# Kernel optimization log

Hardware: AMD Instinct MI355X
Metric: run time of the kernel (lower is better)

Reference implementation:

```python
import jax, jax.numpy as jnp
import numpy as np

B, T, EPROJS, DUNITS, ATT_DIM = 32, 2048, 512, 512, 512
ACONV_CHANS, ACONV_FILT = 32, 100
SCALING = 2.0


def _lin(k, fan_in, fan_out):
    k1, k2 = jax.random.split(k)
    lim = 1.0 / np.sqrt(fan_in)
    w = jax.random.uniform(k1, (fan_in, fan_out), minval=-lim, maxval=lim, dtype=jnp.float32)
    b = jax.random.uniform(k2, (fan_out,), minval=-lim, maxval=lim, dtype=jnp.float32)
    return w, b


def setup_inputs() -> dict:
    key = jax.random.key(0)
    ks = jax.random.split(key, 16)
    W_w, W_b = _lin(ks[0], DUNITS, ATT_DIM)
    V_w, V_b = _lin(ks[1], EPROJS, ATT_DIM)
    U_w, U_b = _lin(ks[2], DUNITS, ATT_DIM)
    g_w, g_b = _lin(ks[3], ATT_DIM, 1)
    K = 2 * ACONV_FILT + 1
    lim = 1.0 / np.sqrt(K)
    conv_w = jax.random.uniform(ks[4], (ACONV_CHANS, 1, K), minval=-lim, maxval=lim, dtype=jnp.float32)
    lim = 1.0 / np.sqrt(ATT_DIM)
    W_ih = jax.random.uniform(ks[5], (4 * ATT_DIM, ACONV_CHANS), minval=-lim, maxval=lim, dtype=jnp.float32)
    W_hh = jax.random.uniform(ks[6], (4 * ATT_DIM, ATT_DIM), minval=-lim, maxval=lim, dtype=jnp.float32)
    b_ih = jax.random.uniform(ks[7], (4 * ATT_DIM,), minval=-lim, maxval=lim, dtype=jnp.float32)
    b_hh = jax.random.uniform(ks[8], (4 * ATT_DIM,), minval=-lim, maxval=lim, dtype=jnp.float32)
    enc_hs_pad = jax.random.normal(ks[9], (B, T, EPROJS), dtype=jnp.float32)
    enc_hs_len = jax.random.randint(ks[10], (B,), T // 2, T + 1, dtype=jnp.int32)
    dec_z = jax.random.normal(ks[11], (B, DUNITS), dtype=jnp.float32)
    att_prev = jax.random.uniform(ks[12], (B, T), dtype=jnp.float32)
    att_h = jax.random.normal(ks[13], (B, ATT_DIM), dtype=jnp.float32)
    att_c = jax.random.normal(ks[14], (B, ATT_DIM), dtype=jnp.float32)
    return dict(enc_hs_pad=enc_hs_pad, enc_hs_len=enc_hs_len, dec_z=dec_z,
                att_prev=att_prev, att_h=att_h, att_c=att_c,
                W_w=W_w, W_b=W_b, V_w=V_w, V_b=V_b, U_w=U_w, U_b=U_b,
                g_w=g_w, g_b=g_b, conv_w=conv_w,
                W_ih=W_ih, W_hh=W_hh, b_ih=b_ih, b_hh=b_hh)


def reference(enc_hs_pad, enc_hs_len, dec_z, att_prev, att_h, att_c,
              W_w, W_b, V_w, V_b, U_w, U_b, g_w, g_b, conv_w,
              W_ih, W_hh, b_ih, b_hh):
    # pre-computed encoder projection: (B, T, att_dim)
    pre = jnp.einsum('bte,ea->bta', enc_hs_pad, V_w) + V_b
    # location conv over previous attention weights: (B, C, T)
    conv = jax.lax.conv_general_dilated(att_prev[:, None, :], conv_w,
                                        window_strides=(1,),
                                        padding=[(ACONV_FILT, ACONV_FILT)],
                                        dimension_numbers=('NCH', 'OIH', 'NCH'))
    feat = jnp.max(jax.nn.relu(conv), axis=-1)  # (B, C): max-pool over time
    # LSTMCell (torch gate order: i, f, g, o)
    gates = feat @ W_ih.T + b_ih + att_h @ W_hh.T + b_hh
    i, f, g, o = jnp.split(gates, 4, axis=-1)
    c_new = jax.nn.sigmoid(f) * att_c + jax.nn.sigmoid(i) * jnp.tanh(g)
    h_new = jax.nn.sigmoid(o) * jnp.tanh(c_new)
    # additive score
    dec_proj = dec_z @ U_w + U_b            # (B, att_dim)
    wh = h_new @ W_w + W_b                  # (B, att_dim)
    e = jnp.tanh(wh[:, None, :] + pre + dec_proj[:, None, :])  # (B, T, att_dim)
    score = jnp.einsum('bta,a->bt', e, g_w[:, 0]) + g_b[0]     # (B, T)
    mask = jnp.arange(T)[None, :] >= enc_hs_len[:, None]
    score = jnp.where(mask, jnp.asarray(-1e30, score.dtype), score)
    w = jax.nn.softmax(SCALING * score, axis=1)
    c_v = jnp.einsum('bte,bt->be', enc_hs_pad, w)  # (B, eprojs)
    return c_v, w, h_new, c_new
```

## Files before the change

kernel.cpp:

```cpp
#include <hip/hip_runtime.h>
#include <math.h>

#define BB 32
#define TT_SEQ 2048
#define EPROJS 512
#define ATT 512
#define NCH 32
#define FILT 100
#define KCONV 201
#define G4 2048

typedef unsigned short ushort_t;
typedef unsigned int uint_t;
typedef __attribute__((ext_vector_type(8))) short bf16x8_t;
typedef __attribute__((ext_vector_type(4))) float f32x4_t;

__device__ inline ushort_t f2bf(float f) {
    uint_t u = __float_as_uint(f);
    uint_t r = (u + 0x7fffu + ((u >> 16) & 1u)) >> 16;
    return (ushort_t)r;
}

__device__ inline float tanh_fast(float x) {
    float e = __expf(2.0f * x);
    return 1.0f - 2.0f / (e + 1.0f);
}

__global__ __launch_bounds__(256) void k_conv(const float* __restrict__ att_prev,
                                              const float* __restrict__ conv_w,
                                              float* __restrict__ feat) {
    int b = blockIdx.x >> 5;
    int c = blockIdx.x & 31;
    __shared__ __align__(16) float row[TT_SEQ + 2 * FILT + 8];
    __shared__ float red[4];
    for (int i = threadIdx.x; i < TT_SEQ + 2 * FILT + 8; i += 256) {
        int t = i - FILT;
        row[i] = (t >= 0 && t < TT_SEQ) ? att_prev[b * TT_SEQ + t] : 0.0f;
    }
    __syncthreads();
    const float* cw = conv_w + c * KCONV;
    int t0 = threadIdx.x * 8;
    float acc[8] = {0.f, 0.f, 0.f, 0.f, 0.f, 0.f, 0.f, 0.f};
    float4 r0 = *(const float4*)(row + t0);
    float4 r1 = *(const float4*)(row + t0 + 4);
    float r[8] = {r0.x, r0.y, r0.z, r0.w, r1.x, r1.y, r1.z, r1.w};
    for (int k = 0; k < 200; k += 8) {
        float4 n0 = *(const float4*)(row + t0 + k + 8);
        float4 n1 = *(const float4*)(row + t0 + k + 12);
        float nn[8] = {n0.x, n0.y, n0.z, n0.w, n1.x, n1.y, n1.z, n1.w};
        #pragma unroll
        for (int kk = 0; kk < 8; ++kk) {
            float w = cw[k + kk];
            #pragma unroll
            for (int i = 0; i < 8; ++i) {
                float rv = (kk + i < 8) ? r[kk + i] : nn[kk + i - 8];
                acc[i] = fmaf(w, rv, acc[i]);
            }
        }
        #pragma unroll
        for (int i = 0; i < 8; ++i) r[i] = nn[i];
    }
    float wlast = cw[200];
    #pragma unroll
    for (int i = 0; i < 8; ++i) acc[i] = fmaf(wlast, r[i], acc[i]);
    float m = 0.0f;
    #pragma unroll
    for (int i = 0; i < 8; ++i) m = fmaxf(m, acc[i]);
    #pragma unroll
    for (int off = 32; off; off >>= 1) m = fmaxf(m, __shfl_xor(m, off, 64));
    if ((threadIdx.x & 63) == 0) red[threadIdx.x >> 6] = m;
    __syncthreads();
    if (threadIdx.x == 0) {
        m = fmaxf(fmaxf(red[0], red[1]), fmaxf(red[2], red[3]));
        feat[b * NCH + c] = m;
    }
}

#define HP 518
__global__ __launch_bounds__(256) void k_gates(const float* __restrict__ feat,
                                               const float* __restrict__ att_h,
                                               const float* __restrict__ W_ih,
                                               const float* __restrict__ W_hh,
                                               const float* __restrict__ b_ih,
                                               const float* __restrict__ b_hh,
                                               float* __restrict__ gates) {
    __shared__ float hsh[32 * HP];
    __shared__ float fsh[32 * 33];
    int tid = threadIdx.x;
    for (int i = tid; i < 32 * 512; i += 256) {
        int r = i >> 9, c = i & 511;
        hsh[r * HP + c] = att_h[i];
    }
    for (int i = tid; i < 1024; i += 256) fsh[(i >> 5) * 33 + (i & 31)] = feat[i];
    __syncthreads();
    int jl = tid >> 5, b = tid & 31;
    int j = blockIdx.x * 8 + jl;
    float acc = b_ih[j] + b_hh[j];
    const float4* wi = (const float4*)(W_ih + (size_t)j * NCH);
    #pragma unroll
    for (int k4 = 0; k4 < 8; ++k4) {
        float4 w = wi[k4];
        const float* f = fsh + b * 33 + k4 * 4;
        acc = fmaf(w.x, f[0], acc);
        acc = fmaf(w.y, f[1], acc);
        acc = fmaf(w.z, f[2], acc);
        acc = fmaf(w.w, f[3], acc);
    }
    const float4* wh = (const float4*)(W_hh + (size_t)j * ATT);
    float a0 = 0.f, a1 = 0.f, a2 = 0.f, a3 = 0.f;
    #pragma unroll 8
    for (int k4 = 0; k4 < 128; ++k4) {
        float4 w = wh[k4];
        float2 h0 = *(const float2*)(hsh + b * HP + k4 * 4);
        float2 h1 = *(const float2*)(hsh + b * HP + k4 * 4 + 2);
        a0 = fmaf(w.x, h0.x, a0);
        a1 = fmaf(w.y, h0.y, a1);
        a2 = fmaf(w.z, h1.x, a2);
        a3 = fmaf(w.w, h1.y, a3);
    }
    gates[(size_t)b * G4 + j] = acc + ((a0 + a1) + (a2 + a3));
}

__global__ __launch_bounds__(256) void k_lstm_elem(const float* __restrict__ gates,
                                                   const float* __restrict__ att_c,
                                                   float* __restrict__ h_out,
                                                   float* __restrict__ c_out) {
    int i = blockIdx.x * 256 + threadIdx.x;
    int b = i >> 9, a = i & 511;
    const float* g = gates + (size_t)b * G4;
    float ig = g[a], fg = g[ATT + a], gg = g[2 * ATT + a], og = g[3 * ATT + a];
    float si = 1.0f / (1.0f + expf(-ig));
    float sf = 1.0f / (1.0f + expf(-fg));
    float so = 1.0f / (1.0f + expf(-og));
    float cn = sf * att_c[i] + si * tanhf(gg);
    float hn = so * tanhf(cn);
    c_out[i] = cn;
    h_out[i] = hn;
}

__global__ __launch_bounds__(256) void k_addvec_par(const float* __restrict__ dec_z,
                                                    const float* __restrict__ h_new,
                                                    const float* __restrict__ U_w,
                                                    const float* __restrict__ W_w,
                                                    float* __restrict__ add_vec) {
    int a0 = blockIdx.x * 32;
    int k0 = blockIdx.y * 64;
    __shared__ float zsh[32 * 65];
    __shared__ float hsh[32 * 65];
    __shared__ float us[64 * 33];
    __shared__ float ws2[64 * 33];
    int tid = threadIdx.x;
    for (int i = tid; i < 2048; i += 256) {
        int b = i >> 6, d = i & 63;
        zsh[b * 65 + d] = dec_z[(size_t)b * ATT + k0 + d];
        hsh[b * 65 + d] = h_new[(size_t)b * ATT + k0 + d];
        int dr = i >> 5, c = i & 31;
        us[dr * 33 + c] = U_w[(size_t)(k0 + dr) * ATT + a0 + c];
        ws2[dr * 33 + c] = W_w[(size_t)(k0 + dr) * ATT + a0 + c];
    }
    __syncthreads();
    int al = tid >> 5, b = tid & 31;
    float acc[4] = {0.f, 0.f, 0.f, 0.f};
    for (int d = 0; d < 64; ++d) {
        float zv = zsh[b * 65 + d];
        float hv = hsh[b * 65 + d];
        #pragma unroll
        for (int m = 0; m < 4; ++m) {
            int a = al + 8 * m;
            acc[m] = fmaf(zv, us[d * 33 + a], acc[m]);
            acc[m] = fmaf(hv, ws2[d * 33 + a], acc[m]);
        }
    }
    #pragma unroll
    for (int m = 0; m < 4; ++m)
        atomicAdd(&add_vec[(size_t)b * ATT + a0 + al + 8 * m], acc[m]);
}

__global__ __launch_bounds__(256) void k_cvt(const float* __restrict__ src,
                                             ushort_t* __restrict__ dst) {
    size_t i = (size_t)blockIdx.x * 256 + threadIdx.x;
    float4 v = ((const float4*)src)[i];
    ushort4 o;
    o.x = f2bf(v.x); o.y = f2bf(v.y); o.z = f2bf(v.z); o.w = f2bf(v.w);
    ((ushort4*)dst)[i] = o;
}

__global__ __launch_bounds__(256) void k_cvtw(const float* __restrict__ vw,
                                              ushort_t* __restrict__ vwt,
                                              const float* __restrict__ U_b,
                                              const float* __restrict__ W_b,
                                              const float* __restrict__ V_b,
                                              float* __restrict__ add_vec) {
    __shared__ float tile[64][65];
    int eb = blockIdx.x * 64, ab = blockIdx.y * 64;
    for (int it = 0; it < 16; ++it) {
        int idx = threadIdx.x + it * 256;
        int r = idx >> 6, c = idx & 63;
        tile[r][c] = vw[(size_t)(eb + r) * ATT + ab + c];
    }
    __syncthreads();
    for (int it = 0; it < 16; ++it) {
        int idx = threadIdx.x + it * 256;
        int r = idx >> 6, c = idx & 63;
        vwt[(size_t)(ab + r) * EPROJS + eb + c] = f2bf(tile[c][r]);
    }
    int blk = blockIdx.y * 8 + blockIdx.x;
    int i = blk * 256 + threadIdx.x;
    int a = i & 511;
    add_vec[i] = U_b[a] + W_b[a] + V_b[a];
}

__global__ __launch_bounds__(512, 2) void k_gemm_score2(
        const ushort_t* __restrict__ Abf,
        const ushort_t* __restrict__ Btbf,
        const float* __restrict__ add_vec,
        const float* __restrict__ g_w,
        const int* __restrict__ lens,
        float* __restrict__ score) {
    int mtile = blockIdx.x;
    int b = mtile >> 4;
    int t0 = (mtile & 15) * 128;
    if (t0 >= lens[b]) return;

    __shared__ __align__(16) ushort_t sA[128 * 64];
    __shared__ __align__(16) ushort_t sB[512 * 64];

    int tid = threadIdx.x;
    int lane = tid & 63;
    int wave = tid >> 6;
    int wm = wave >> 2, wn = wave & 3;
    int q = lane >> 4, l15 = lane & 15;

    const ushort_t* Ag = Abf + (size_t)mtile * 128 * EPROJS;

    f32x4_t acc[4][8];
    #pragma unroll
    for (int i = 0; i < 4; ++i)
        #pragma unroll
        for (int j = 0; j < 8; ++j) acc[i][j] = (f32x4_t){0.f, 0.f, 0.f, 0.f};

    for (int kc = 0; kc < 8; ++kc) {
        __syncthreads();
        #pragma unroll
        for (int it = 0; it < 2; ++it) {
            int g = tid + it * 512;
            int m = g >> 3;
            int kq = g & 7;
            int kqs = kq ^ (m & 7);
            __builtin_amdgcn_global_load_lds(
                (const __attribute__((address_space(1))) void*)(Ag + (size_t)m * EPROJS + kc * 64 + kqs * 8),
                (__attribute__((address_space(3))) void*)(sA + g * 8), 16, 0, 0);
        }
        #pragma unroll
        for (int it = 0; it < 8; ++it) {
            int g = tid + it * 512;
            int n = g >> 3;
            int kq = g & 7;
            int kqs = kq ^ (n & 7);
            __builtin_amdgcn_global_load_lds(
                (const __attribute__((address_space(1))) void*)(Btbf + (size_t)n * EPROJS + kc * 64 + kqs * 8),
                (__attribute__((address_space(3))) void*)(sB + g * 8), 16, 0, 0);
        }
        __syncthreads();
        #pragma unroll
        for (int s = 0; s < 2; ++s) {
            bf16x8_t af[4], bfr[8];
            int kq = s * 4 + q;
            #pragma unroll
            for (int i = 0; i < 4; ++i) {
                int m = wm * 64 + i * 16 + l15;
                af[i] = *(const bf16x8_t*)(sA + (m * 8 + (kq ^ (m & 7))) * 8);
            }
            #pragma unroll
            for (int j = 0; j < 8; ++j) {
                int n = wn * 128 + j * 16 + l15;
                bfr[j] = *(const bf16x8_t*)(sB + (n * 8 + (kq ^ (n & 7))) * 8);
            }
            #pragma unroll
            for (int i = 0; i < 4; ++i)
                #pragma unroll
                for (int j = 0; j < 8; ++j)
                    acc[i][j] = __builtin_amdgcn_mfma_f32_16x16x32_bf16(af[i], bfr[j], acc[i][j], 0, 0, 0);
        }
    }

    float g8[8], av8[8];
    #pragma unroll
    for (int j = 0; j < 8; ++j) {
        int a = wn * 128 + j * 16 + l15;
        g8[j] = g_w[a];
        av8[j] = add_vec[b * ATT + a];
    }
    float s_ir[4][4];
    #pragma unroll
    for (int i = 0; i < 4; ++i) {
        #pragma unroll
        for (int r = 0; r < 4; ++r) {
            float s = 0.0f;
            #pragma unroll
            for (int j = 0; j < 8; ++j) {
                float x = acc[i][j][r] + av8[j];
                s = fmaf(g8[j], tanh_fast(x), s);
            }
            s_ir[i][r] = s;
        }
    }
    #pragma unroll
    for (int off = 8; off; off >>= 1) {
        #pragma unroll
        for (int i = 0; i < 4; ++i)
            #pragma unroll
            for (int r = 0; r < 4; ++r)
                s_ir[i][r] += __shfl_xor(s_ir[i][r], off, 16);
    }
    __syncthreads();
    float* sred = (float*)sA;
    if (tid < 128) sred[tid] = 0.0f;
    __syncthreads();
    if (l15 == 0) {
        #pragma unroll
        for (int i = 0; i < 4; ++i)
            #pragma unroll
            for (int r = 0; r < 4; ++r)
                atomicAdd(&sred[wm * 64 + i * 16 + q * 4 + r], s_ir[i][r]);
    }
    __syncthreads();
    if (tid < 128) score[b * TT_SEQ + t0 + tid] = sred[tid];
}

__global__ __launch_bounds__(256) void k_softmax(const float* __restrict__ score,
                                                 const int* __restrict__ lens,
                                                 float* __restrict__ w_out,
                                                 float* __restrict__ c_v) {
    int b = blockIdx.x;
    int len = lens[b];
    __shared__ float red[4];
    float vals[8];
    float m = -INFINITY;
    #pragma unroll
    for (int i = 0; i < 8; ++i) {
        int t = threadIdx.x + i * 256;
        float s = (t < len) ? 2.0f * score[b * TT_SEQ + t] : -INFINITY;
        vals[i] = s;
        m = fmaxf(m, s);
    }
    #pragma unroll
    for (int off = 32; off; off >>= 1) m = fmaxf(m, __shfl_xor(m, off, 64));
    if ((threadIdx.x & 63) == 0) red[threadIdx.x >> 6] = m;
    __syncthreads();
    m = fmaxf(fmaxf(red[0], red[1]), fmaxf(red[2], red[3]));
    __syncthreads();
    float sum = 0.0f;
    #pragma unroll
    for (int i = 0; i < 8; ++i) {
        float e = expf(vals[i] - m);
        vals[i] = e;
        sum += e;
    }
    #pragma unroll
    for (int off = 32; off; off >>= 1) sum += __shfl_xor(sum, off, 64);
    if ((threadIdx.x & 63) == 0) red[threadIdx.x >> 6] = sum;
    __syncthreads();
    sum = red[0] + red[1] + red[2] + red[3];
    float inv = 1.0f / sum;
    #pragma unroll
    for (int i = 0; i < 8; ++i) w_out[b * TT_SEQ + threadIdx.x + i * 256] = vals[i] * inv;
    for (int i = threadIdx.x; i < EPROJS; i += 256) c_v[b * EPROJS + i] = 0.0f;
}

__global__ __launch_bounds__(256) void k_ctx_bf(const ushort_t* __restrict__ encb,
                                                const float* __restrict__ w,
                                                const int* __restrict__ lens,
                                                float* __restrict__ c_v) {
    int b = blockIdx.y;
    int t0 = blockIdx.x * 64;
    if (t0 >= lens[b]) return;
    __shared__ float wsh[64];
    if (threadIdx.x < 64) wsh[threadIdx.x] = w[b * TT_SEQ + t0 + threadIdx.x];
    __syncthreads();
    const uint_t* base = (const uint_t*)(encb + ((size_t)b * TT_SEQ + t0) * EPROJS);
    float a0 = 0.f, a1 = 0.f;
    for (int t = 0; t < 64; ++t) {
        uint_t u = base[t * 256 + threadIdx.x];
        float lo = __uint_as_float(u << 16);
        float hi = __uint_as_float(u & 0xffff0000u);
        a0 = fmaf(wsh[t], lo, a0);
        a1 = fmaf(wsh[t], hi, a1);
    }
    atomicAdd(&c_v[b * EPROJS + 2 * threadIdx.x], a0);
    atomicAdd(&c_v[b * EPROJS + 2 * threadIdx.x + 1], a1);
}

__global__ __launch_bounds__(256) void k_lstm(const float* __restrict__ feat,
                                              const float* __restrict__ att_h,
                                              const float* __restrict__ att_c,
                                              const float* __restrict__ W_ih,
                                              const float* __restrict__ W_hh,
                                              const float* __restrict__ b_ih,
                                              const float* __restrict__ b_hh,
                                              float* __restrict__ h_out,
                                              float* __restrict__ c_out) {
    int b = blockIdx.x;
    __shared__ float fsh[NCH];
    __shared__ float hsh[ATT];
    __shared__ float gsh[G4];
    if (threadIdx.x < NCH) fsh[threadIdx.x] = feat[b * NCH + threadIdx.x];
    for (int i = threadIdx.x; i < ATT; i += 256) hsh[i] = att_h[b * ATT + i];
    __syncthreads();
    for (int j = threadIdx.x; j < G4; j += 256) {
        float acc = b_ih[j] + b_hh[j];
        const float* wi = W_ih + (size_t)j * NCH;
        #pragma unroll
        for (int c = 0; c < NCH; ++c) acc = fmaf(fsh[c], wi[c], acc);
        const float* wh = W_hh + (size_t)j * ATT;
        for (int a = 0; a < ATT; a += 4) {
            float4 w4 = *(const float4*)(wh + a);
            acc = fmaf(hsh[a + 0], w4.x, acc);
            acc = fmaf(hsh[a + 1], w4.y, acc);
            acc = fmaf(hsh[a + 2], w4.z, acc);
            acc = fmaf(hsh[a + 3], w4.w, acc);
        }
        gsh[j] = acc;
    }
    __syncthreads();
    for (int a = threadIdx.x; a < ATT; a += 256) {
        float ig = gsh[a], fg = gsh[ATT + a], gg = gsh[2 * ATT + a], og = gsh[3 * ATT + a];
        float si = 1.0f / (1.0f + expf(-ig));
        float sf = 1.0f / (1.0f + expf(-fg));
        float so = 1.0f / (1.0f + expf(-og));
        float cn = sf * att_c[b * ATT + a] + si * tanhf(gg);
        float hn = so * tanhf(cn);
        c_out[b * ATT + a] = cn;
        h_out[b * ATT + a] = hn;
    }
}

__global__ __launch_bounds__(256) void k_addvec(const float* __restrict__ dec_z,
                                                const float* __restrict__ h_new,
                                                const float* __restrict__ U_w,
                                                const float* __restrict__ U_b,
                                                const float* __restrict__ W_w,
                                                const float* __restrict__ W_b,
                                                const float* __restrict__ V_b,
                                                float* __restrict__ add_vec) {
    int b = blockIdx.x;
    __shared__ float zsh[ATT];
    __shared__ float hsh[ATT];
    for (int i = threadIdx.x; i < ATT; i += 256) {
        zsh[i] = dec_z[b * ATT + i];
        hsh[i] = h_new[b * ATT + i];
    }
    __syncthreads();
    for (int a = threadIdx.x; a < ATT; a += 256) {
        float acc = U_b[a] + W_b[a] + V_b[a];
        for (int d = 0; d < ATT; ++d) {
            acc = fmaf(zsh[d], U_w[(size_t)d * ATT + a], acc);
            acc = fmaf(hsh[d], W_w[(size_t)d * ATT + a], acc);
        }
        add_vec[b * ATT + a] = acc;
    }
}

#define TTILE 16
#define SR 516
__global__ __launch_bounds__(256) void k_score(const float* __restrict__ enc,
                                               const float* __restrict__ V_w,
                                               const float* __restrict__ add_vec,
                                               const float* __restrict__ g_w,
                                               const float* __restrict__ g_b,
                                               const int* __restrict__ lens,
                                               float* __restrict__ score) {
    int b = blockIdx.y;
    int t0 = blockIdx.x * TTILE;
    int len = lens[b];
    if (t0 >= len) return;
    __shared__ float enc_t[TTILE * SR];
    __shared__ float ash[ATT];
    __shared__ float gwsh[ATT];
    const float* src = enc + ((size_t)b * TT_SEQ + t0) * EPROJS;
    for (int i = threadIdx.x; i < TTILE * 128; i += 256) {
        int r = i >> 7, c4 = (i & 127) << 2;
        *(float4*)(enc_t + r * SR + c4) = *(const float4*)(src + (size_t)r * EPROJS + c4);
    }
    for (int i = threadIdx.x; i < ATT; i += 256) {
        ash[i] = add_vec[b * ATT + i];
        gwsh[i] = g_w[i];
    }
    __syncthreads();
    int t = threadIdx.x >> 4;
    int al = threadIdx.x & 15;
    const float* er = enc_t + t * SR;
    float sc = 0.0f;
    #pragma unroll
    for (int c = 0; c < 2; ++c) {
        float4 acc0 = {0, 0, 0, 0}, acc1 = {0, 0, 0, 0}, acc2 = {0, 0, 0, 0}, acc3 = {0, 0, 0, 0};
        int abase = c * 256 + al * 4;
        const float* vp = V_w + abase;
        for (int e = 0; e < EPROJS; ++e) {
            float s = er[e];
            const float* rowp = vp + (size_t)e * ATT;
            float4 w0 = *(const float4*)(rowp);
            float4 w1 = *(const float4*)(rowp + 64);
            float4 w2 = *(const float4*)(rowp + 128);
            float4 w3 = *(const float4*)(rowp + 192);
            acc0.x = fmaf(s, w0.x, acc0.x); acc0.y = fmaf(s, w0.y, acc0.y);
            acc0.z = fmaf(s, w0.z, acc0.z); acc0.w = fmaf(s, w0.w, acc0.w);
            acc1.x = fmaf(s, w1.x, acc1.x); acc1.y = fmaf(s, w1.y, acc1.y);
            acc1.z = fmaf(s, w1.z, acc1.z); acc1.w = fmaf(s, w1.w, acc1.w);
            acc2.x = fmaf(s, w2.x, acc2.x); acc2.y = fmaf(s, w2.y, acc2.y);
            acc2.z = fmaf(s, w2.z, acc2.z); acc2.w = fmaf(s, w2.w, acc2.w);
            acc3.x = fmaf(s, w3.x, acc3.x); acc3.y = fmaf(s, w3.y, acc3.y);
            acc3.z = fmaf(s, w3.z, acc3.z); acc3.w = fmaf(s, w3.w, acc3.w);
        }
        float av[16] = {acc0.x, acc0.y, acc0.z, acc0.w,
                        acc1.x, acc1.y, acc1.z, acc1.w,
                        acc2.x, acc2.y, acc2.z, acc2.w,
                        acc3.x, acc3.y, acc3.z, acc3.w};
        #pragma unroll
        for (int k = 0; k < 16; ++k) {
            int a = abase + (k >> 2) * 64 + (k & 3);
            sc = fmaf(gwsh[a], tanhf(av[k] + ash[a]), sc);
        }
    }
    #pragma unroll
    for (int off = 8; off; off >>= 1) sc += __shfl_xor(sc, off, 16);
    if (al == 0) score[b * TT_SEQ + t0 + t] = sc + g_b[0];
}

__global__ __launch_bounds__(256) void k_ctx(const float* __restrict__ enc,
                                             const float* __restrict__ w,
                                             const int* __restrict__ lens,
                                             float* __restrict__ c_v) {
    int b = blockIdx.y;
    int t0 = blockIdx.x * 128;
    if (t0 >= lens[b]) return;
    __shared__ float wsh[128];
    if (threadIdx.x < 128) wsh[threadIdx.x] = w[b * TT_SEQ + t0 + threadIdx.x];
    __syncthreads();
    float a0 = 0.0f, a1 = 0.0f;
    const float* base = enc + ((size_t)b * TT_SEQ + t0) * EPROJS;
    for (int t = 0; t < 128; ++t) {
        float wt = wsh[t];
        a0 = fmaf(wt, base[(size_t)t * EPROJS + threadIdx.x], a0);
        a1 = fmaf(wt, base[(size_t)t * EPROJS + threadIdx.x + 256], a1);
    }
    atomicAdd(&c_v[b * EPROJS + threadIdx.x], a0);
    atomicAdd(&c_v[b * EPROJS + threadIdx.x + 256], a1);
}

extern "C" void kernel_launch(void* const* d_in, const int* in_sizes, int n_in,
                              void* d_out, int out_size, void* d_ws, size_t ws_size,
                              hipStream_t stream) {
    const float* enc      = (const float*)d_in[0];
    const int*   lens     = (const int*)d_in[1];
    const float* dec_z    = (const float*)d_in[2];
    const float* att_prev = (const float*)d_in[3];
    const float* att_h    = (const float*)d_in[4];
    const float* att_c    = (const float*)d_in[5];
    const float* W_w      = (const float*)d_in[6];
    const float* W_b      = (const float*)d_in[7];
    const float* V_w      = (const float*)d_in[8];
    const float* V_b      = (const float*)d_in[9];
    const float* U_w      = (const float*)d_in[10];
    const float* U_b      = (const float*)d_in[11];
    const float* g_w      = (const float*)d_in[12];
    const float* g_b      = (const float*)d_in[13];
    const float* conv_w   = (const float*)d_in[14];
    const float* W_ih     = (const float*)d_in[15];
    const float* W_hh     = (const float*)d_in[16];
    const float* b_ih     = (const float*)d_in[17];
    const float* b_hh     = (const float*)d_in[18];

    float* out   = (float*)d_out;
    float* c_v   = out;
    float* w_out = out + BB * EPROJS;
    float* h_out = w_out + BB * TT_SEQ;
    float* c_out = h_out + BB * ATT;

    const size_t ENC_N = (size_t)BB * TT_SEQ * EPROJS;
    const size_t need = ENC_N * 2 + (size_t)ATT * EPROJS * 2 +
                        (size_t)(1024 + BB * ATT + BB * TT_SEQ + BB * G4) * sizeof(float);

    if (ws_size >= need) {
        ushort_t* encb = (ushort_t*)d_ws;
        ushort_t* vwt  = encb + ENC_N;
        float* feat    = (float*)(vwt + (size_t)ATT * EPROJS);
        float* add_vec = feat + 1024;
        float* score   = add_vec + BB * ATT;
        float* gates   = score + BB * TT_SEQ;

        k_cvt<<<dim3(ENC_N / 4 / 256), dim3(256), 0, stream>>>(enc, encb);
        k_cvtw<<<dim3(8, 8), dim3(256), 0, stream>>>(V_w, vwt, U_b, W_b, V_b, add_vec);
        k_conv<<<dim3(BB * NCH), dim3(256), 0, stream>>>(att_prev, conv_w, feat);
        k_gates<<<dim3(G4 / 8), dim3(256), 0, stream>>>(feat, att_h, W_ih, W_hh,
                                                        b_ih, b_hh, gates);
        k_lstm_elem<<<dim3(64), dim3(256), 0, stream>>>(gates, att_c, h_out, c_out);
        k_addvec_par<<<dim3(16, 8), dim3(256), 0, stream>>>(dec_z, h_out, U_w, W_w, add_vec);
        k_gemm_score2<<<dim3(512), dim3(512), 0, stream>>>(encb, vwt, add_vec, g_w,
                                                           lens, score);
        k_softmax<<<dim3(BB), dim3(256), 0, stream>>>(score, lens, w_out, c_v);
        k_ctx_bf<<<dim3(32, BB), dim3(256), 0, stream>>>(encb, w_out, lens, c_v);
    } else {
        float* ws      = (float*)d_ws;
        float* feat    = ws;
        float* add_vec = ws + 1024;
        float* score   = ws + 1024 + BB * ATT;

        k_conv<<<dim3(BB * NCH), dim3(256), 0, stream>>>(att_prev, conv_w, feat);
        k_lstm<<<dim3(BB), dim3(256), 0, stream>>>(feat, att_h, att_c, W_ih, W_hh,
                                                   b_ih, b_hh, h_out, c_out);
        k_addvec<<<dim3(BB), dim3(256), 0, stream>>>(dec_z, h_out, U_w, U_b, W_w, W_b,
                                                     V_b, add_vec);
        k_score<<<dim3(TT_SEQ / TTILE, BB), dim3(256), 0, stream>>>(enc, V_w, add_vec,
                                                                    g_w, g_b, lens, score);
        k_softmax<<<dim3(BB), dim3(256), 0, stream>>>(score, lens, w_out, c_v);
        k_ctx<<<dim3(16, BB), dim3(256), 0, stream>>>(enc, w_out, lens, c_v);
    }
}
```

Measured before the change: 348.5 us.

## Drop bf16 encoder copy, convert in GEMM loader, fuse small preprocessing kernels

Removes the separate pass that converts the whole encoder tensor to bf16. The score GEMM now reads fp32 encoder rows and converts them to bf16 in registers while filling shared memory, and the context kernel reads fp32 directly. The conv, V_w transpose and bias init are merged into one launch, and the LSTM elementwise step is folded into the add-vector kernel. This saves a large write and re-read of the encoder tensor plus several launches. In exchange the GEMM A-tile fill uses synchronous register loads instead of async global-to-LDS loads, the context kernel reads twice as many bytes, and the LSTM activations are recomputed by every block.

Result: faster. 326.5 us (-6.3%).

```diff
diff --git a/kernel.cpp b/kernel.cpp
--- a/kernel.cpp
+++ b/kernel.cpp
@@ -26,53 +26,80 @@
     return 1.0f - 2.0f / (e + 1.0f);
 }
 
-__global__ __launch_bounds__(256) void k_conv(const float* __restrict__ att_prev,
-                                              const float* __restrict__ conv_w,
-                                              float* __restrict__ feat) {
-    int b = blockIdx.x >> 5;
-    int c = blockIdx.x & 31;
-    __shared__ __align__(16) float row[TT_SEQ + 2 * FILT + 8];
+__global__ __launch_bounds__(256) void k_pre(const float* __restrict__ att_prev,
+                                             const float* __restrict__ conv_w,
+                                             float* __restrict__ feat,
+                                             const float* __restrict__ vw,
+                                             ushort_t* __restrict__ vwt,
+                                             const float* __restrict__ U_b,
+                                             const float* __restrict__ W_b,
+                                             const float* __restrict__ V_b,
+                                             float* __restrict__ add_vec) {
+    __shared__ __align__(16) float shbuf[64 * 65];
     __shared__ float red[4];
-    for (int i = threadIdx.x; i < TT_SEQ + 2 * FILT + 8; i += 256) {
-        int t = i - FILT;
-        row[i] = (t >= 0 && t < TT_SEQ) ? att_prev[b * TT_SEQ + t] : 0.0f;
-    }
-    __syncthreads();
-    const float* cw = conv_w + c * KCONV;
-    int t0 = threadIdx.x * 8;
-    float acc[8] = {0.f, 0.f, 0.f, 0.f, 0.f, 0.f, 0.f, 0.f};
-    float4 r0 = *(const float4*)(row + t0);
-    float4 r1 = *(const float4*)(row + t0 + 4);
-    float r[8] = {r0.x, r0.y, r0.z, r0.w, r1.x, r1.y, r1.z, r1.w};
-    for (int k = 0; k < 200; k += 8) {
-        float4 n0 = *(const float4*)(row + t0 + k + 8);
-        float4 n1 = *(const float4*)(row + t0 + k + 12);
-        float nn[8] = {n0.x, n0.y, n0.z, n0.w, n1.x, n1.y, n1.z, n1.w};
-        #pragma unroll
-        for (int kk = 0; kk < 8; ++kk) {
-            float w = cw[k + kk];
-            #pragma unroll
-            for (int i = 0; i < 8; ++i) {
-                float rv = (kk + i < 8) ? r[kk + i] : nn[kk + i - 8];
-                acc[i] = fmaf(w, rv, acc[i]);
+    if (blockIdx.x < 1024) {
+        int b = blockIdx.x >> 5;
+        int c = blockIdx.x & 31;
+        float* row = shbuf;
+        for (int i = threadIdx.x; i < TT_SEQ + 2 * FILT + 8; i += 256) {
+            int t = i - FILT;
+            row[i] = (t >= 0 && t < TT_SEQ) ? att_prev[b * TT_SEQ + t] : 0.0f;
+        }
+        __syncthreads();
+        const float* cw = conv_w + c * KCONV;
+        int t0 = threadIdx.x * 8;
+        float acc[8] = {0.f, 0.f, 0.f, 0.f, 0.f, 0.f, 0.f, 0.f};
+        float4 r0 = *(const float4*)(row + t0);
+        float4 r1 = *(const float4*)(row + t0 + 4);
+        float r[8] = {r0.x, r0.y, r0.z, r0.w, r1.x, r1.y, r1.z, r1.w};
+        for (int k = 0; k < 200; k += 8) {
+            float4 n0 = *(const float4*)(row + t0 + k + 8);
+            float4 n1 = *(const float4*)(row + t0 + k + 12);
+            float nn[8] = {n0.x, n0.y, n0.z, n0.w, n1.x, n1.y, n1.z, n1.w};
+            #pragma unroll
+            for (int kk = 0; kk < 8; ++kk) {
+                float w = cw[k + kk];
+                #pragma unroll
+                for (int i = 0; i < 8; ++i) {
+                    float rv = (kk + i < 8) ? r[kk + i] : nn[kk + i - 8];
+                    acc[i] = fmaf(w, rv, acc[i]);
+                }
             }
-        }
-        #pragma unroll
-        for (int i = 0; i < 8; ++i) r[i] = nn[i];
-    }
-    float wlast = cw[200];
-    #pragma unroll
-    for (int i = 0; i < 8; ++i) acc[i] = fmaf(wlast, r[i], acc[i]);
-    float m = 0.0f;
-    #pragma unroll
-    for (int i = 0; i < 8; ++i) m = fmaxf(m, acc[i]);
-    #pragma unroll
-    for (int off = 32; off; off >>= 1) m = fmaxf(m, __shfl_xor(m, off, 64));
-    if ((threadIdx.x & 63) == 0) red[threadIdx.x >> 6] = m;
-    __syncthreads();
-    if (threadIdx.x == 0) {
-        m = fmaxf(fmaxf(red[0], red[1]), fmaxf(red[2], red[3]));
-        feat[b * NCH + c] = m;
+            #pragma unroll
+            for (int i = 0; i < 8; ++i) r[i] = nn[i];
+        }
+        float wlast = cw[200];
+        #pragma unroll
+        for (int i = 0; i < 8; ++i) acc[i] = fmaf(wlast, r[i], acc[i]);
+        float m = 0.0f;
+        #pragma unroll
+        for (int i = 0; i < 8; ++i) m = fmaxf(m, acc[i]);
+        #pragma unroll
+        for (int off = 32; off; off >>= 1) m = fmaxf(m, __shfl_xor(m, off, 64));
+        if ((threadIdx.x & 63) == 0) red[threadIdx.x >> 6] = m;
+        __syncthreads();
+        if (threadIdx.x == 0) {
+            m = fmaxf(fmaxf(red[0], red[1]), fmaxf(red[2], red[3]));
+            feat[b * NCH + c] = m;
+        }
+    } else {
+        int id = blockIdx.x - 1024;
+        int eb = (id & 7) * 64, ab = (id >> 3) * 64;
+        float (*tile)[65] = (float (*)[65])shbuf;
+        for (int it = 0; it < 16; ++it) {
+            int idx = threadIdx.x + it * 256;
+            int r = idx >> 6, c = idx & 63;
+            tile[r][c] = vw[(size_t)(eb + r) * ATT + ab + c];
+        }
+        __syncthreads();
+        for (int it = 0; it < 16; ++it) {
+            int idx = threadIdx.x + it * 256;
+            int r = idx >> 6, c = idx & 63;
+            vwt[(size_t)(ab + r) * EPROJS + eb + c] = f2bf(tile[c][r]);
+        }
+        int i = id * 256 + threadIdx.x;
+        int a = i & 511;
+        add_vec[i] = U_b[a] + W_b[a] + V_b[a];
     }
 }
 
@@ -121,28 +148,14 @@
     gates[(size_t)b * G4 + j] = acc + ((a0 + a1) + (a2 + a3));
 }
 
-__global__ __launch_bounds__(256) void k_lstm_elem(const float* __restrict__ gates,
-                                                   const float* __restrict__ att_c,
-                                                   float* __restrict__ h_out,
-                                                   float* __restrict__ c_out) {
-    int i = blockIdx.x * 256 + threadIdx.x;
-    int b = i >> 9, a = i & 511;
-    const float* g = gates + (size_t)b * G4;
-    float ig = g[a], fg = g[ATT + a], gg = g[2 * ATT + a], og = g[3 * ATT + a];
-    float si = 1.0f / (1.0f + expf(-ig));
-    float sf = 1.0f / (1.0f + expf(-fg));
-    float so = 1.0f / (1.0f + expf(-og));
-    float cn = sf * att_c[i] + si * tanhf(gg);
-    float hn = so * tanhf(cn);
-    c_out[i] = cn;
-    h_out[i] = hn;
-}
-
-__global__ __launch_bounds__(256) void k_addvec_par(const float* __restrict__ dec_z,
-                                                    const float* __restrict__ h_new,
-                                                    const float* __restrict__ U_w,
-                                                    const float* __restrict__ W_w,
-                                                    float* __restrict__ add_vec) {
+__global__ __launch_bounds__(256) void k_hz(const float* __restrict__ gates,
+                                            const float* __restrict__ att_c,
+                                            const float* __restrict__ dec_z,
+                                            const float* __restrict__ U_w,
+                                            const float* __restrict__ W_w,
+                                            float* __restrict__ h_out,
+                                            float* __restrict__ c_out,
+                                            float* __restrict__ add_vec) {
     int a0 = blockIdx.x * 32;
     int k0 = blockIdx.y * 64;
     __shared__ float zsh[32 * 65];
@@ -152,8 +165,17 @@
     int tid = threadIdx.x;
     for (int i = tid; i < 2048; i += 256) {
         int b = i >> 6, d = i & 63;
-        zsh[b * 65 + d] = dec_z[(size_t)b * ATT + k0 + d];
-        hsh[b * 65 + d] = h_new[(size_t)b * ATT + k0 + d];
+        int idx = b * ATT + k0 + d;
+        const float* g = gates + (size_t)b * G4 + k0 + d;
+        float ig = g[0], fg = g[ATT], gg = g[2 * ATT], og = g[3 * ATT];
+        float si = 1.0f / (1.0f + expf(-ig));
+        float sf = 1.0f / (1.0f + expf(-fg));
+        float so = 1.0f / (1.0f + expf(-og));
+        float cn = sf * att_c[idx] + si * tanhf(gg);
+        float hn = so * tanhf(cn);
+        hsh[b * 65 + d] = hn;
+        if (blockIdx.x == 0) { c_out[idx] = cn; h_out[idx] = hn; }
+        zsh[b * 65 + d] = dec_z[idx];
         int dr = i >> 5, c = i & 31;
         us[dr * 33 + c] = U_w[(size_t)(k0 + dr) * ATT + a0 + c];
         ws2[dr * 33 + c] = W_w[(size_t)(k0 + dr) * ATT + a0 + c];
@@ -176,42 +198,8 @@
         atomicAdd(&add_vec[(size_t)b * ATT + a0 + al + 8 * m], acc[m]);
 }
 
-__global__ __launch_bounds__(256) void k_cvt(const float* __restrict__ src,
-                                             ushort_t* __restrict__ dst) {
-    size_t i = (size_t)blockIdx.x * 256 + threadIdx.x;
-    float4 v = ((const float4*)src)[i];
-    ushort4 o;
-    o.x = f2bf(v.x); o.y = f2bf(v.y); o.z = f2bf(v.z); o.w = f2bf(v.w);
-    ((ushort4*)dst)[i] = o;
-}
-
-__global__ __launch_bounds__(256) void k_cvtw(const float* __restrict__ vw,
-                                              ushort_t* __restrict__ vwt,
-                                              const float* __restrict__ U_b,
-                                              const float* __restrict__ W_b,
-                                              const float* __restrict__ V_b,
-                                              float* __restrict__ add_vec) {
-    __shared__ float tile[64][65];
-    int eb = blockIdx.x * 64, ab = blockIdx.y * 64;
-    for (int it = 0; it < 16; ++it) {
-        int idx = threadIdx.x + it * 256;
-        int r = idx >> 6, c = idx & 63;
-        tile[r][c] = vw[(size_t)(eb + r) * ATT + ab + c];
-    }
-    __syncthreads();
-    for (int it = 0; it < 16; ++it) {
-        int idx = threadIdx.x + it * 256;
-        int r = idx >> 6, c = idx & 63;
-        vwt[(size_t)(ab + r) * EPROJS + eb + c] = f2bf(tile[c][r]);
-    }
-    int blk = blockIdx.y * 8 + blockIdx.x;
-    int i = blk * 256 + threadIdx.x;
-    int a = i & 511;
-    add_vec[i] = U_b[a] + W_b[a] + V_b[a];
-}
-
 __global__ __launch_bounds__(512, 2) void k_gemm_score2(
-        const ushort_t* __restrict__ Abf,
+        const float* __restrict__ enc,
         const ushort_t* __restrict__ Btbf,
         const float* __restrict__ add_vec,
         const float* __restrict__ g_w,
@@ -231,7 +219,7 @@
     int wm = wave >> 2, wn = wave & 3;
     int q = lane >> 4, l15 = lane & 15;
 
-    const ushort_t* Ag = Abf + (size_t)mtile * 128 * EPROJS;
+    const float* Ag = enc + (size_t)mtile * 128 * EPROJS;
 
     f32x4_t acc[4][8];
     #pragma unroll
@@ -241,16 +229,6 @@
 
     for (int kc = 0; kc < 8; ++kc) {
         __syncthreads();
-        #pragma unroll
-        for (int it = 0; it < 2; ++it) {
-            int g = tid + it * 512;
-            int m = g >> 3;
-            int kq = g & 7;
-            int kqs = kq ^ (m & 7);
-            __builtin_amdgcn_global_load_lds(
-                (const __attribute__((address_space(1))) void*)(Ag + (size_t)m * EPROJS + kc * 64 + kqs * 8),
-                (__attribute__((address_space(3))) void*)(sA + g * 8), 16, 0, 0);
-        }
         #pragma unroll
         for (int it = 0; it < 8; ++it) {
             int g = tid + it * 512;
@@ -260,6 +238,22 @@
             __builtin_amdgcn_global_load_lds(
                 (const __attribute__((address_space(1))) void*)(Btbf + (size_t)n * EPROJS + kc * 64 + kqs * 8),
                 (__attribute__((address_space(3))) void*)(sB + g * 8), 16, 0, 0);
+        }
+        #pragma unroll
+        for (int it = 0; it < 2; ++it) {
+            int g = tid + it * 512;
+            int m = g >> 3;
+            int kq = g & 7;
+            int kqs = kq ^ (m & 7);
+            const float* src = Ag + (size_t)m * EPROJS + kc * 64 + kqs * 8;
+            float4 v0 = *(const float4*)(src);
+            float4 v1 = *(const float4*)(src + 4);
+            bf16x8_t o;
+            o[0] = (short)f2bf(v0.x); o[1] = (short)f2bf(v0.y);
+            o[2] = (short)f2bf(v0.z); o[3] = (short)f2bf(v0.w);
+            o[4] = (short)f2bf(v1.x); o[5] = (short)f2bf(v1.y);
+            o[6] = (short)f2bf(v1.z); o[7] = (short)f2bf(v1.w);
+            *(bf16x8_t*)(sA + g * 8) = o;
         }
         __syncthreads();
         #pragma unroll
@@ -368,27 +362,56 @@
     for (int i = threadIdx.x; i < EPROJS; i += 256) c_v[b * EPROJS + i] = 0.0f;
 }
 
-__global__ __launch_bounds__(256) void k_ctx_bf(const ushort_t* __restrict__ encb,
-                                                const float* __restrict__ w,
-                                                const int* __restrict__ lens,
-                                                float* __restrict__ c_v) {
+__global__ __launch_bounds__(256) void k_ctx64(const float* __restrict__ enc,
+                                               const float* __restrict__ w,
+                                               const int* __restrict__ lens,
+                                               float* __restrict__ c_v) {
     int b = blockIdx.y;
     int t0 = blockIdx.x * 64;
     if (t0 >= lens[b]) return;
     __shared__ float wsh[64];
     if (threadIdx.x < 64) wsh[threadIdx.x] = w[b * TT_SEQ + t0 + threadIdx.x];
     __syncthreads();
-    const uint_t* base = (const uint_t*)(encb + ((size_t)b * TT_SEQ + t0) * EPROJS);
+    const float* base = enc + ((size_t)b * TT_SEQ + t0) * EPROJS;
     float a0 = 0.f, a1 = 0.f;
     for (int t = 0; t < 64; ++t) {
-        uint_t u = base[t * 256 + threadIdx.x];
-        float lo = __uint_as_float(u << 16);
-        float hi = __uint_as_float(u & 0xffff0000u);
-        a0 = fmaf(wsh[t], lo, a0);
-        a1 = fmaf(wsh[t], hi, a1);
-    }
-    atomicAdd(&c_v[b * EPROJS + 2 * threadIdx.x], a0);
-    atomicAdd(&c_v[b * EPROJS + 2 * threadIdx.x + 1], a1);
+        float wt = wsh[t];
+        a0 = fmaf(wt, base[(size_t)t * EPROJS + threadIdx.x], a0);
+        a1 = fmaf(wt, base[(size_t)t * EPROJS + threadIdx.x + 256], a1);
+    }
+    atomicAdd(&c_v[b * EPROJS + threadIdx.x], a0);
+    atomicAdd(&c_v[b * EPROJS + threadIdx.x + 256], a1);
+}
+
+__global__ __launch_bounds__(256) void k_conv_fb(const float* __restrict__ att_prev,
+                                                 const float* __restrict__ conv_w,
+                                                 float* __restrict__ feat) {
+    int b = blockIdx.x >> 5;
+    int c = blockIdx.x & 31;
+    __shared__ float row[TT_SEQ + 2 * FILT];
+    __shared__ float wsh[KCONV];
+    __shared__ float red[4];
+    for (int i = threadIdx.x; i < TT_SEQ + 2 * FILT; i += 256) {
+        int t = i - FILT;
+        row[i] = (t >= 0 && t < TT_SEQ) ? att_prev[b * TT_SEQ + t] : 0.0f;
+    }
+    for (int i = threadIdx.x; i < KCONV; i += 256) wsh[i] = conv_w[c * KCONV + i];
+    __syncthreads();
+    float m = 0.0f;
+    for (int t = threadIdx.x; t < TT_SEQ; t += 256) {
+        float s = 0.0f;
+        #pragma unroll 4
+        for (int k = 0; k < KCONV; ++k) s = fmaf(wsh[k], row[t + k], s);
+        m = fmaxf(m, s);
+    }
+    #pragma unroll
+    for (int off = 32; off; off >>= 1) m = fmaxf(m, __shfl_xor(m, off, 64));
+    if ((threadIdx.x & 63) == 0) red[threadIdx.x >> 6] = m;
+    __syncthreads();
+    if (threadIdx.x == 0) {
+        m = fmaxf(fmaxf(red[0], red[1]), fmaxf(red[2], red[3]));
+        feat[b * NCH + c] = m;
+    }
 }
 
 __global__ __launch_bounds__(256) void k_lstm(const float* __restrict__ feat,
@@ -525,27 +548,6 @@
     #pragma unroll
     for (int off = 8; off; off >>= 1) sc += __shfl_xor(sc, off, 16);
     if (al == 0) score[b * TT_SEQ + t0 + t] = sc + g_b[0];
-}
-
-__global__ __launch_bounds__(256) void k_ctx(const float* __restrict__ enc,
-                                             const float* __restrict__ w,
-                                             const int* __restrict__ lens,
-                                             float* __restrict__ c_v) {
-    int b = blockIdx.y;
-    int t0 = blockIdx.x * 128;
-    if (t0 >= lens[b]) return;
-    __shared__ float wsh[128];
-    if (threadIdx.x < 128) wsh[threadIdx.x] = w[b * TT_SEQ + t0 + threadIdx.x];
-    __syncthreads();
-    float a0 = 0.0f, a1 = 0.0f;
-    const float* base = enc + ((size_t)b * TT_SEQ + t0) * EPROJS;
-    for (int t = 0; t < 128; ++t) {
-        float wt = wsh[t];
-        a0 = fmaf(wt, base[(size_t)t * EPROJS + threadIdx.x], a0);
-        a1 = fmaf(wt, base[(size_t)t * EPROJS + threadIdx.x + 256], a1);
-    }
-    atomicAdd(&c_v[b * EPROJS + threadIdx.x], a0);
-    atomicAdd(&c_v[b * EPROJS + threadIdx.x + 256], a1);
 }
 
 extern "C" void kernel_launch(void* const* d_in, const int* in_sizes, int n_in,
@@ -577,36 +579,33 @@
     float* h_out = w_out + BB * TT_SEQ;
     float* c_out = h_out + BB * ATT;
 
-    const size_t ENC_N = (size_t)BB * TT_SEQ * EPROJS;
-    const size_t need = ENC_N * 2 + (size_t)ATT * EPROJS * 2 +
+    const size_t need = (size_t)ATT * EPROJS * 2 +
                         (size_t)(1024 + BB * ATT + BB * TT_SEQ + BB * G4) * sizeof(float);
 
     if (ws_size >= need) {
-        ushort_t* encb = (ushort_t*)d_ws;
-        ushort_t* vwt  = encb + ENC_N;
+        ushort_t* vwt  = (ushort_t*)d_ws;
         float* feat    = (float*)(vwt + (size_t)ATT * EPROJS);
         float* add_vec = feat + 1024;
         float* score   = add_vec + BB * ATT;
         float* gates   = score + BB * TT_SEQ;
 
-        k_cvt<<<dim3(ENC_N / 4 / 256), dim3(256), 0, stream>>>(enc, encb);
-        k_cvtw<<<dim3(8, 8), dim3(256), 0, stream>>>(V_w, vwt, U_b, W_b, V_b, add_vec);
-        k_conv<<<dim3(BB * NCH), dim3(256), 0, stream>>>(att_prev, conv_w, feat);
+        k_pre<<<dim3(1024 + 64), dim3(256), 0, stream>>>(att_prev, conv_w, feat,
+                                                         V_w, vwt, U_b, W_b, V_b, add_vec);
         k_gates<<<dim3(G4 / 8), dim3(256), 0, stream>>>(feat, att_h, W_ih, W_hh,
                                                         b_ih, b_hh, gates);
-        k_lstm_elem<<<dim3(64), dim3(256), 0, stream>>>(gates, att_c, h_out, c_out);
-        k_addvec_par<<<dim3(16, 8), dim3(256), 0, stream>>>(dec_z, h_out, U_w, W_w, add_vec);
-        k_gemm_score2<<<dim3(512), dim3(512), 0, stream>>>(encb, vwt, add_vec, g_w,
+        k_hz<<<dim3(16, 8), dim3(256), 0, stream>>>(gates, att_c, dec_z, U_w, W_w,
+                                                    h_out, c_out, add_vec);
+        k_gemm_score2<<<dim3(512), dim3(512), 0, stream>>>(enc, vwt, add_vec, g_w,
                                                            lens, score);
         k_softmax<<<dim3(BB), dim3(256), 0, stream>>>(score, lens, w_out, c_v);
-        k_ctx_bf<<<dim3(32, BB), dim3(256), 0, stream>>>(encb, w_out, lens, c_v);
+        k_ctx64<<<dim3(32, BB), dim3(256), 0, stream>>>(enc, w_out, lens, c_v);
     } else {
         float* ws      = (float*)d_ws;
         float* feat    = ws;
         float* add_vec = ws + 1024;
         float* score   = ws + 1024 + BB * ATT;
 
-        k_conv<<<dim3(BB * NCH), dim3(256), 0, stream>>>(att_prev, conv_w, feat);
+        k_conv_fb<<<dim3(BB * NCH), dim3(256), 0, stream>>>(att_prev, conv_w, feat);
         k_lstm<<<dim3(BB), dim3(256), 0, stream>>>(feat, att_h, att_c, W_ih, W_hh,
                                                    b_ih, b_hh, h_out, c_out);
         k_addvec<<<dim3(BB), dim3(256), 0, stream>>>(dec_z, h_out, U_w, U_b, W_w, W_b,
@@ -614,6 +613,6 @@
         k_score<<<dim3(TT_SEQ / TTILE, BB), dim3(256), 0, stream>>>(enc, V_w, add_vec,
                                                                     g_w, g_b, lens, score);
         k_softmax<<<dim3(BB), dim3(256), 0, stream>>>(score, lens, w_out, c_v);
-        k_ctx<<<dim3(16, BB), dim3(256), 0, stream>>>(enc, w_out, lens, c_v);
-    }
-}
+        k_ctx64<<<dim3(32, BB), dim3(256), 0, stream>>>(enc, w_out, lens, c_v);
+    }
+}
```
